# Kernel optimization log

Measured on AMD Instinct MI355X. Metric: run time of the kernel, lower is better.

The kernel has to match this reference:

```python
import jax, jax.numpy as jnp
import numpy as np

EMBED_DIM = 128
NUM_HEADS = 4
WIN = (7, 7)
N = WIN[0] * WIN[1]  # 49
NW = 64              # windows per image
B = 128              # batch of images
SCALE = (EMBED_DIM // NUM_HEADS) ** -0.5


def _relative_position_index():
    coords = np.stack(np.meshgrid(np.arange(WIN[0]), np.arange(WIN[1]), indexing='ij'))
    cf = coords.reshape(2, -1)                       # [2, N]
    rel = cf[:, :, None] - cf[:, None, :]            # [2, N, N]
    rel = rel.transpose(1, 2, 0).astype(np.int64)    # [N, N, 2]
    rel[..., 0] += WIN[0] - 1
    rel[..., 0] *= 2 * WIN[1] - 1
    rel[..., 1] += WIN[1] - 1
    return rel.sum(-1).reshape(-1)                   # [N*N]


def setup_inputs() -> dict:
    key = jax.random.key(0)
    ks = jax.random.split(key, 6)
    C = EMBED_DIM
    x = jax.random.normal(ks[0], (NW * B, N, C), dtype=jnp.float32)
    mask = jnp.zeros((NW, N, N), dtype=jnp.float32)
    qkv_w = jax.random.normal(ks[1], (3 * C, C), dtype=jnp.float32) * (C ** -0.5)
    qkv_b = jnp.zeros((3 * C,), dtype=jnp.float32)
    proj_w = jax.random.normal(ks[2], (C, C), dtype=jnp.float32) * (C ** -0.5)
    proj_b = jnp.zeros((C,), dtype=jnp.float32)
    bias_table = jax.random.normal(ks[3], ((2 * WIN[0] - 1) * (2 * WIN[1] - 1), NUM_HEADS), dtype=jnp.float32) * 0.02
    rel_index = jnp.asarray(_relative_position_index(), dtype=jnp.int32)
    return {"x": x, "mask": mask, "qkv_w": qkv_w, "qkv_b": qkv_b,
            "proj_w": proj_w, "proj_b": proj_b, "bias_table": bias_table,
            "rel_index": rel_index}


def reference(x, mask, qkv_w, qkv_b, proj_w, proj_b, bias_table, rel_index):
    nwb, n, c = x.shape
    nh, ch = NUM_HEADS, c // NUM_HEADS
    qkv = x @ qkv_w.T + qkv_b                               # [nwb, n, 3c]
    qkv = qkv.reshape(nwb, n, 3, nh, ch)
    q, k, v = (jnp.moveaxis(qkv, (2, 3), (0, 2))[i] for i in range(3))  # each [nwb, nh, n, ch]
    attn = jnp.einsum('whik,whjk->whij', q * SCALE, k)      # [nwb, nh, n, n]
    # relative position bias: gather then reshape to [1, nh, n, n]
    bias = bias_table[rel_index].reshape(n, n, nh).transpose(2, 0, 1)[None]
    attn = attn + bias
    if mask is not None:
        nw = mask.shape[0]
        attn = attn.reshape(nwb // nw, nw, nh, n, n) + mask[None, :, None]
        attn = attn.reshape(nwb, nh, n, n)
    attn = jax.nn.softmax(attn, axis=-1)
    out = jnp.einsum('whij,whjd->whid', attn, v)            # [nwb, nh, n, ch]
    out = out.transpose(0, 2, 1, 3).reshape(nwb, n, c)
    return out @ proj_w.T + proj_b
```

## Files before the change

kernel.cpp:

```cpp
#include <hip/hip_runtime.h>

typedef __bf16 bf16x8 __attribute__((ext_vector_type(8)));
typedef float  f32x4  __attribute__((ext_vector_type(4)));

#define NTOK  49
#define CDIM  128
#define QK_SCALE 0.17677669529663687f

#define XS 136
#define QS 264
#define VS 72
#define PS 64

#define WQKV_OFF  0
#define WPROJ_OFF 98304
#define BIASF_OFF 131072

__global__ void prep_kernel(const float* __restrict__ qkv_w,
                            const float* __restrict__ proj_w,
                            const float* __restrict__ bias_table,
                            const int*   __restrict__ rel_index,
                            __bf16* __restrict__ wqkv,
                            __bf16* __restrict__ wproj,
                            float*  __restrict__ biasf) {
    int t = blockIdx.x * 256 + threadIdx.x;
    if (t < 384 * 128) wqkv[t]  = (__bf16)qkv_w[t];
    if (t < 128 * 128) wproj[t] = (__bf16)proj_w[t];
    if (t < 4 * 2401) {
        int h = t / 2401, ij = t % 2401;
        biasf[t] = bias_table[rel_index[ij] * 4 + h];
    }
}

__launch_bounds__(256, 2)
__global__ void winattn_kernel(const float* __restrict__ x,
                               const float* __restrict__ mask,
                               const float* __restrict__ qkv_b,
                               const float* __restrict__ proj_b,
                               const __bf16* __restrict__ wqkv,
                               const __bf16* __restrict__ wproj,
                               const float* __restrict__ biasf,
                               float* __restrict__ out) {
    __shared__ __bf16 lds_x[64 * XS];
    __shared__ __bf16 lds_qkv[64 * QS];
    __shared__ __bf16 lds_vt[128 * VS];
    __bf16* lds_p = lds_qkv;

    const int tid  = threadIdx.x;
    const int w    = blockIdx.x;
    const int wave = tid >> 6;
    const int lane = tid & 63;
    const int quad = lane >> 4;
    const int l16  = lane & 15;

    {
        int row = tid >> 2;
        int c0  = (tid & 3) * 32;
        __align__(16) __bf16 tmp[32];
        if (row < NTOK) {
            const float4* src = (const float4*)(x + ((size_t)w * NTOK + row) * CDIM + c0);
            #pragma unroll
            for (int i = 0; i < 8; ++i) {
                float4 f = src[i];
                tmp[i*4+0] = (__bf16)f.x; tmp[i*4+1] = (__bf16)f.y;
                tmp[i*4+2] = (__bf16)f.z; tmp[i*4+3] = (__bf16)f.w;
            }
        } else {
            #pragma unroll
            for (int i = 0; i < 32; ++i) tmp[i] = (__bf16)0.0f;
        }
        bf16x8* dst = (bf16x8*)&lds_x[row * XS + c0];
        #pragma unroll
        for (int i = 0; i < 4; ++i) dst[i] = *(bf16x8*)&tmp[i*8];
    }
    __syncthreads();

    #pragma unroll
    for (int half = 0; half < 2; ++half) {
        f32x4 acc[3][4];
        #pragma unroll
        for (int a = 0; a < 3; ++a)
            #pragma unroll
            for (int b = 0; b < 4; ++b) acc[a][b] = (f32x4){0.f,0.f,0.f,0.f};

        #pragma unroll
        for (int kt = 0; kt < 4; ++kt) {
            bf16x8 a4[4];
            #pragma unroll
            for (int mt = 0; mt < 4; ++mt)
                a4[mt] = *(bf16x8*)&lds_x[(mt*16 + l16) * XS + kt*32 + quad*8];
            #pragma unroll
            for (int ntl = 0; ntl < 3; ++ntl) {
                int o = (wave*6 + half*3 + ntl) * 16 + l16;
                bf16x8 bf = *(const bf16x8*)(wqkv + (size_t)o * CDIM + kt*32 + quad*8);
                #pragma unroll
                for (int mt = 0; mt < 4; ++mt)
                    acc[ntl][mt] = __builtin_amdgcn_mfma_f32_16x16x32_bf16(
                        a4[mt], bf, acc[ntl][mt], 0, 0, 0);
            }
        }
        #pragma unroll
        for (int ntl = 0; ntl < 3; ++ntl) {
            int o = (wave*6 + half*3 + ntl) * 16 + l16;
            float b = qkv_b[o];
            #pragma unroll
            for (int mt = 0; mt < 4; ++mt) {
                #pragma unroll
                for (int r = 0; r < 4; ++r) {
                    int row = mt*16 + quad*4 + r;
                    float v = acc[ntl][mt][r] + b;
                    if (o < 128)       lds_qkv[row * QS + o] = (__bf16)(v * QK_SCALE);
                    else if (o < 256)  lds_qkv[row * QS + o] = (__bf16)v;
                    else               lds_vt[(o - 256) * VS + row] = (__bf16)v;
                }
            }
        }
    }
    __syncthreads();

    {
        const int h = wave;
        bf16x8 bk[4];
        #pragma unroll
        for (int nt = 0; nt < 4; ++nt)
            bk[nt] = *(bf16x8*)&lds_qkv[(nt*16 + l16) * QS + 128 + h*32 + quad*8];

        f32x4 s[4][4];
        #pragma unroll
        for (int mt = 0; mt < 4; ++mt) {
            bf16x8 aq = *(bf16x8*)&lds_qkv[(mt*16 + l16) * QS + h*32 + quad*8];
            #pragma unroll
            for (int nt = 0; nt < 4; ++nt) {
                f32x4 z = (f32x4){0.f,0.f,0.f,0.f};
                s[mt][nt] = __builtin_amdgcn_mfma_f32_16x16x32_bf16(aq, bk[nt], z, 0, 0, 0);
            }
        }

        const float* bh = biasf + h * 2401;
        const float* mh = mask + (size_t)(w & 63) * 2401;
        #pragma unroll
        for (int mt = 0; mt < 4; ++mt) {
            #pragma unroll
            for (int r = 0; r < 4; ++r) {
                int i = mt*16 + quad*4 + r;
                float v[4];
                #pragma unroll
                for (int nt = 0; nt < 4; ++nt) {
                    int j = nt*16 + l16;
                    float t = s[mt][nt][r];
                    if (j < NTOK) { if (i < NTOK) t += bh[i*49 + j] + mh[i*49 + j]; }
                    else t = -1e30f;
                    v[nt] = t;
                }
                float mx = fmaxf(fmaxf(v[0], v[1]), fmaxf(v[2], v[3]));
                mx = fmaxf(mx, __shfl_xor(mx, 1, 64));
                mx = fmaxf(mx, __shfl_xor(mx, 2, 64));
                mx = fmaxf(mx, __shfl_xor(mx, 4, 64));
                mx = fmaxf(mx, __shfl_xor(mx, 8, 64));
                float e[4], sum = 0.f;
                #pragma unroll
                for (int nt = 0; nt < 4; ++nt) { e[nt] = __expf(v[nt] - mx); sum += e[nt]; }
                sum += __shfl_xor(sum, 1, 64);
                sum += __shfl_xor(sum, 2, 64);
                sum += __shfl_xor(sum, 4, 64);
                sum += __shfl_xor(sum, 8, 64);
                float inv = 1.0f / sum;
                #pragma unroll
                for (int nt = 0; nt < 4; ++nt) s[mt][nt][r] = e[nt] * inv;
            }
        }
        __syncthreads();
        #pragma unroll
        for (int mt = 0; mt < 4; ++mt)
            #pragma unroll
            for (int r = 0; r < 4; ++r)
                #pragma unroll
                for (int nt = 0; nt < 4; ++nt)
                    lds_p[((h << 6) + mt*16 + quad*4 + r) * PS + nt*16 + l16] =
                        (__bf16)s[mt][nt][r];
    }
    __syncthreads();

    {
        const int h = wave;
        bf16x8 bv[2][2];
        #pragma unroll
        for (int nv = 0; nv < 2; ++nv)
            #pragma unroll
            for (int kt = 0; kt < 2; ++kt)
                bv[nv][kt] = *(bf16x8*)&lds_vt[(h*32 + nv*16 + l16) * VS + kt*32 + quad*8];

        f32x4 oacc[4][2];
        #pragma unroll
        for (int a = 0; a < 4; ++a)
            #pragma unroll
            for (int b = 0; b < 2; ++b) oacc[a][b] = (f32x4){0.f,0.f,0.f,0.f};

        #pragma unroll
        for (int mt = 0; mt < 4; ++mt)
            #pragma unroll
            for (int kt = 0; kt < 2; ++kt) {
                bf16x8 ap = *(bf16x8*)&lds_p[((h << 6) + mt*16 + l16) * PS + kt*32 + quad*8];
                #pragma unroll
                for (int nv = 0; nv < 2; ++nv)
                    oacc[mt][nv] = __builtin_amdgcn_mfma_f32_16x16x32_bf16(
                        ap, bv[nv][kt], oacc[mt][nv], 0, 0, 0);
            }

        #pragma unroll
        for (int mt = 0; mt < 4; ++mt)
            #pragma unroll
            for (int nv = 0; nv < 2; ++nv)
                #pragma unroll
                for (int r = 0; r < 4; ++r) {
                    int row = mt*16 + quad*4 + r;
                    lds_x[row * XS + h*32 + nv*16 + l16] = (__bf16)oacc[mt][nv][r];
                }
    }
    __syncthreads();

    #pragma unroll
    for (int ntl = 0; ntl < 2; ++ntl) {
        int o = (wave*2 + ntl) * 16 + l16;
        f32x4 acc[4];
        #pragma unroll
        for (int a = 0; a < 4; ++a) acc[a] = (f32x4){0.f,0.f,0.f,0.f};
        #pragma unroll
        for (int kt = 0; kt < 4; ++kt) {
            bf16x8 bf = *(const bf16x8*)(wproj + (size_t)o * CDIM + kt*32 + quad*8);
            #pragma unroll
            for (int mt = 0; mt < 4; ++mt) {
                bf16x8 af = *(bf16x8*)&lds_x[(mt*16 + l16) * XS + kt*32 + quad*8];
                acc[mt] = __builtin_amdgcn_mfma_f32_16x16x32_bf16(af, bf, acc[mt], 0, 0, 0);
            }
        }
        float pb = proj_b[o];
        #pragma unroll
        for (int mt = 0; mt < 4; ++mt)
            #pragma unroll
            for (int r = 0; r < 4; ++r) {
                int row = mt*16 + quad*4 + r;
                if (row < NTOK)
                    out[((size_t)w * NTOK + row) * CDIM + o] = acc[mt][r] + pb;
            }
    }
}

extern "C" void kernel_launch(void* const* d_in, const int* in_sizes, int n_in,
                              void* d_out, int out_size, void* d_ws, size_t ws_size,
                              hipStream_t stream) {
    const float* x          = (const float*)d_in[0];
    const float* mask       = (const float*)d_in[1];
    const float* qkv_w      = (const float*)d_in[2];
    const float* qkv_b      = (const float*)d_in[3];
    const float* proj_w     = (const float*)d_in[4];
    const float* proj_b     = (const float*)d_in[5];
    const float* bias_table = (const float*)d_in[6];
    const int*   rel_index  = (const int*)d_in[7];

    __bf16* wqkv  = (__bf16*)((char*)d_ws + WQKV_OFF);
    __bf16* wproj = (__bf16*)((char*)d_ws + WPROJ_OFF);
    float*  biasf = (float*)((char*)d_ws + BIASF_OFF);

    int nwb = in_sizes[0] / (NTOK * CDIM);

    prep_kernel<<<192, 256, 0, stream>>>(qkv_w, proj_w, bias_table, rel_index,
                                         wqkv, wproj, biasf);
    winattn_kernel<<<nwb, 256, 0, stream>>>(x, mask, qkv_b, proj_b,
                                            wqkv, wproj, biasf, (float*)d_out);
}
```

Before: 639.2 us.

## Keep Q/K/P in registers, premerge bias+mask in bf16, raise occupancy

Restructures the window-attention kernel so each wave computes its head's Q and K projections transposed and keeps them in registers as MFMA operands. The scores are computed as K·Q^T with 16x16x16 MFMAs, so the softmax probabilities feed the P·V MFMA straight from registers. This removes the large lds_qkv buffer and the LDS round trips for Q, K and P. The prep kernel now builds a padded bf16 table that folds the relative-position bias, mask and -inf padding together per window, head and position, replacing the separate fp32 bias and mask loads. Launch bounds rise to 4 blocks per CU, which risks register pressure and costs a larger, bf16-rounded bias/mask table.

```diff
diff --git a/kernel.cpp b/kernel.cpp
--- a/kernel.cpp
+++ b/kernel.cpp
@@ -1,6 +1,8 @@
 #include <hip/hip_runtime.h>
 
 typedef __bf16 bf16x8 __attribute__((ext_vector_type(8)));
+typedef __bf16 bf16x4 __attribute__((ext_vector_type(4)));
+typedef short  short4v __attribute__((ext_vector_type(4)));
 typedef float  f32x4  __attribute__((ext_vector_type(4)));
 
 #define NTOK  49
@@ -8,47 +10,60 @@
 #define QK_SCALE 0.17677669529663687f
 
 #define XS 136
-#define QS 264
 #define VS 72
-#define PS 64
 
 #define WQKV_OFF  0
 #define WPROJ_OFF 98304
-#define BIASF_OFF 131072
+#define BM_OFF    131072
+
+#define MFMA32(A,B,C) __builtin_amdgcn_mfma_f32_16x16x32_bf16(A,B,C,0,0,0)
+#define MFMA16(A,B,C) __builtin_amdgcn_mfma_f32_16x16x16bf16_1k(A,B,C,0,0,0)
 
 __global__ void prep_kernel(const float* __restrict__ qkv_w,
                             const float* __restrict__ proj_w,
                             const float* __restrict__ bias_table,
                             const int*   __restrict__ rel_index,
+                            const float* __restrict__ mask,
                             __bf16* __restrict__ wqkv,
                             __bf16* __restrict__ wproj,
-                            float*  __restrict__ biasf) {
+                            __bf16* __restrict__ bm) {
     int t = blockIdx.x * 256 + threadIdx.x;
     if (t < 384 * 128) wqkv[t]  = (__bf16)qkv_w[t];
     if (t < 128 * 128) wproj[t] = (__bf16)proj_w[t];
-    if (t < 4 * 2401) {
-        int h = t / 2401, ij = t % 2401;
-        biasf[t] = bias_table[rel_index[ij] * 4 + h];
-    }
-}
-
-__launch_bounds__(256, 2)
+    {
+        int i  = t & 63;
+        int j  = (t >> 6) & 63;
+        int h  = (t >> 12) & 3;
+        int wq = t >> 14;
+        float v;
+        if (j >= NTOK)      v = -1e30f;
+        else if (i >= NTOK) v = 0.0f;
+        else v = bias_table[rel_index[i * 49 + j] * 4 + h] + mask[wq * 2401 + i * 49 + j];
+        bm[t] = (__bf16)v;
+    }
+}
+
+static __device__ __forceinline__ short4v cvt_scale(f32x4 v, float b, float sc) {
+    bf16x4 r;
+    #pragma unroll
+    for (int i = 0; i < 4; ++i) r[i] = (__bf16)((v[i] + b) * sc);
+    return __builtin_bit_cast(short4v, r);
+}
+
+__launch_bounds__(256, 4)
 __global__ void winattn_kernel(const float* __restrict__ x,
-                               const float* __restrict__ mask,
                                const float* __restrict__ qkv_b,
                                const float* __restrict__ proj_b,
                                const __bf16* __restrict__ wqkv,
                                const __bf16* __restrict__ wproj,
-                               const float* __restrict__ biasf,
+                               const __bf16* __restrict__ bm,
                                float* __restrict__ out) {
     __shared__ __bf16 lds_x[64 * XS];
-    __shared__ __bf16 lds_qkv[64 * QS];
     __shared__ __bf16 lds_vt[128 * VS];
-    __bf16* lds_p = lds_qkv;
 
     const int tid  = threadIdx.x;
     const int w    = blockIdx.x;
-    const int wave = tid >> 6;
+    const int h    = tid >> 6;
     const int lane = tid & 63;
     const int quad = lane >> 4;
     const int l16  = lane & 15;
@@ -75,153 +90,166 @@
     }
     __syncthreads();
 
-    #pragma unroll
-    for (int half = 0; half < 2; ++half) {
-        f32x4 acc[3][4];
-        #pragma unroll
-        for (int a = 0; a < 3; ++a)
+    short4v qf[2][4], kf[2][4];
+
+    #pragma unroll
+    for (int sub = 0; sub < 3; ++sub) {
+        const int obase = sub * 128 + h * 32;
+        f32x4 acc[2][4];
+        #pragma unroll
+        for (int a = 0; a < 2; ++a)
             #pragma unroll
             for (int b = 0; b < 4; ++b) acc[a][b] = (f32x4){0.f,0.f,0.f,0.f};
 
         #pragma unroll
         for (int kt = 0; kt < 4; ++kt) {
-            bf16x8 a4[4];
-            #pragma unroll
-            for (int mt = 0; mt < 4; ++mt)
-                a4[mt] = *(bf16x8*)&lds_x[(mt*16 + l16) * XS + kt*32 + quad*8];
-            #pragma unroll
-            for (int ntl = 0; ntl < 3; ++ntl) {
-                int o = (wave*6 + half*3 + ntl) * 16 + l16;
-                bf16x8 bf = *(const bf16x8*)(wqkv + (size_t)o * CDIM + kt*32 + quad*8);
-                #pragma unroll
-                for (int mt = 0; mt < 4; ++mt)
-                    acc[ntl][mt] = __builtin_amdgcn_mfma_f32_16x16x32_bf16(
-                        a4[mt], bf, acc[ntl][mt], 0, 0, 0);
-            }
-        }
-        #pragma unroll
-        for (int ntl = 0; ntl < 3; ++ntl) {
-            int o = (wave*6 + half*3 + ntl) * 16 + l16;
-            float b = qkv_b[o];
-            #pragma unroll
-            for (int mt = 0; mt < 4; ++mt) {
-                #pragma unroll
-                for (int r = 0; r < 4; ++r) {
-                    int row = mt*16 + quad*4 + r;
-                    float v = acc[ntl][mt][r] + b;
-                    if (o < 128)       lds_qkv[row * QS + o] = (__bf16)(v * QK_SCALE);
-                    else if (o < 256)  lds_qkv[row * QS + o] = (__bf16)v;
-                    else               lds_vt[(o - 256) * VS + row] = (__bf16)v;
+            bf16x8 aw[2];
+            #pragma unroll
+            for (int mt = 0; mt < 2; ++mt)
+                aw[mt] = *(const bf16x8*)(wqkv + (size_t)(obase + mt*16 + l16) * CDIM + kt*32 + quad*8);
+            #pragma unroll
+            for (int nt = 0; nt < 4; ++nt) {
+                bf16x8 xb = *(bf16x8*)&lds_x[(nt*16 + l16) * XS + kt*32 + quad*8];
+                #pragma unroll
+                for (int mt = 0; mt < 2; ++mt)
+                    acc[mt][nt] = MFMA32(aw[mt], xb, acc[mt][nt]);
+            }
+        }
+
+        float bias[2][4];
+        #pragma unroll
+        for (int mt = 0; mt < 2; ++mt)
+            #pragma unroll
+            for (int r = 0; r < 4; ++r)
+                bias[mt][r] = qkv_b[obase + mt*16 + quad*4 + r];
+
+        if (sub == 0) {
+            #pragma unroll
+            for (int mt = 0; mt < 2; ++mt)
+                #pragma unroll
+                for (int nt = 0; nt < 4; ++nt) {
+                    bf16x4 r4;
+                    #pragma unroll
+                    for (int r = 0; r < 4; ++r)
+                        r4[r] = (__bf16)((acc[mt][nt][r] + bias[mt][r]) * QK_SCALE);
+                    qf[mt][nt] = __builtin_bit_cast(short4v, r4);
                 }
-            }
-        }
-    }
+        } else if (sub == 1) {
+            #pragma unroll
+            for (int mt = 0; mt < 2; ++mt)
+                #pragma unroll
+                for (int nt = 0; nt < 4; ++nt) {
+                    bf16x4 r4;
+                    #pragma unroll
+                    for (int r = 0; r < 4; ++r)
+                        r4[r] = (__bf16)(acc[mt][nt][r] + bias[mt][r]);
+                    kf[mt][nt] = __builtin_bit_cast(short4v, r4);
+                }
+        } else {
+            #pragma unroll
+            for (int mt = 0; mt < 2; ++mt)
+                #pragma unroll
+                for (int nt = 0; nt < 4; ++nt)
+                    #pragma unroll
+                    for (int r = 0; r < 4; ++r)
+                        lds_vt[(h*32 + mt*16 + quad*4 + r) * VS + nt*16 + l16] =
+                            (__bf16)(acc[mt][nt][r] + bias[mt][r]);
+        }
+    }
+
+    f32x4 s[4][4];
+    #pragma unroll
+    for (int jt = 0; jt < 4; ++jt)
+        #pragma unroll
+        for (int it = 0; it < 4; ++it) {
+            f32x4 z = (f32x4){0.f,0.f,0.f,0.f};
+            z = MFMA16(kf[0][jt], qf[0][it], z);
+            s[jt][it] = MFMA16(kf[1][jt], qf[1][it], z);
+        }
+
+    {
+        const __bf16* bmw = bm + (((size_t)(w & 63) * 4 + h) << 12);
+        #pragma unroll
+        for (int jt = 0; jt < 4; ++jt)
+            #pragma unroll
+            for (int r = 0; r < 4; ++r) {
+                int j = jt*16 + quad*4 + r;
+                #pragma unroll
+                for (int it = 0; it < 4; ++it)
+                    s[jt][it][r] += (float)bmw[j*64 + it*16 + l16];
+            }
+    }
+
+    short4v pf[4][4];
+    #pragma unroll
+    for (int it = 0; it < 4; ++it) {
+        float mx = -1e30f;
+        #pragma unroll
+        for (int jt = 0; jt < 4; ++jt)
+            #pragma unroll
+            for (int r = 0; r < 4; ++r) mx = fmaxf(mx, s[jt][it][r]);
+        mx = fmaxf(mx, __shfl_xor(mx, 16, 64));
+        mx = fmaxf(mx, __shfl_xor(mx, 32, 64));
+        float sum = 0.f;
+        #pragma unroll
+        for (int jt = 0; jt < 4; ++jt)
+            #pragma unroll
+            for (int r = 0; r < 4; ++r) {
+                float e = __expf(s[jt][it][r] - mx);
+                s[jt][it][r] = e;
+                sum += e;
+            }
+        sum += __shfl_xor(sum, 16, 64);
+        sum += __shfl_xor(sum, 32, 64);
+        float inv = 1.0f / sum;
+        #pragma unroll
+        for (int jt = 0; jt < 4; ++jt) {
+            bf16x4 r4;
+            #pragma unroll
+            for (int r = 0; r < 4; ++r) r4[r] = (__bf16)(s[jt][it][r] * inv);
+            pf[jt][it] = __builtin_bit_cast(short4v, r4);
+        }
+    }
+
     __syncthreads();
 
     {
-        const int h = wave;
-        bf16x8 bk[4];
-        #pragma unroll
-        for (int nt = 0; nt < 4; ++nt)
-            bk[nt] = *(bf16x8*)&lds_qkv[(nt*16 + l16) * QS + 128 + h*32 + quad*8];
-
-        f32x4 s[4][4];
-        #pragma unroll
-        for (int mt = 0; mt < 4; ++mt) {
-            bf16x8 aq = *(bf16x8*)&lds_qkv[(mt*16 + l16) * QS + h*32 + quad*8];
-            #pragma unroll
-            for (int nt = 0; nt < 4; ++nt) {
-                f32x4 z = (f32x4){0.f,0.f,0.f,0.f};
-                s[mt][nt] = __builtin_amdgcn_mfma_f32_16x16x32_bf16(aq, bk[nt], z, 0, 0, 0);
-            }
-        }
-
-        const float* bh = biasf + h * 2401;
-        const float* mh = mask + (size_t)(w & 63) * 2401;
-        #pragma unroll
-        for (int mt = 0; mt < 4; ++mt) {
-            #pragma unroll
-            for (int r = 0; r < 4; ++r) {
-                int i = mt*16 + quad*4 + r;
-                float v[4];
-                #pragma unroll
-                for (int nt = 0; nt < 4; ++nt) {
-                    int j = nt*16 + l16;
-                    float t = s[mt][nt][r];
-                    if (j < NTOK) { if (i < NTOK) t += bh[i*49 + j] + mh[i*49 + j]; }
-                    else t = -1e30f;
-                    v[nt] = t;
-                }
-                float mx = fmaxf(fmaxf(v[0], v[1]), fmaxf(v[2], v[3]));
-                mx = fmaxf(mx, __shfl_xor(mx, 1, 64));
-                mx = fmaxf(mx, __shfl_xor(mx, 2, 64));
-                mx = fmaxf(mx, __shfl_xor(mx, 4, 64));
-                mx = fmaxf(mx, __shfl_xor(mx, 8, 64));
-                float e[4], sum = 0.f;
-                #pragma unroll
-                for (int nt = 0; nt < 4; ++nt) { e[nt] = __expf(v[nt] - mx); sum += e[nt]; }
-                sum += __shfl_xor(sum, 1, 64);
-                sum += __shfl_xor(sum, 2, 64);
-                sum += __shfl_xor(sum, 4, 64);
-                sum += __shfl_xor(sum, 8, 64);
-                float inv = 1.0f / sum;
-                #pragma unroll
-                for (int nt = 0; nt < 4; ++nt) s[mt][nt][r] = e[nt] * inv;
-            }
-        }
-        __syncthreads();
-        #pragma unroll
-        for (int mt = 0; mt < 4; ++mt)
-            #pragma unroll
-            for (int r = 0; r < 4; ++r)
-                #pragma unroll
-                for (int nt = 0; nt < 4; ++nt)
-                    lds_p[((h << 6) + mt*16 + quad*4 + r) * PS + nt*16 + l16] =
-                        (__bf16)s[mt][nt][r];
+        short4v bv[2][4];
+        #pragma unroll
+        for (int nv = 0; nv < 2; ++nv)
+            #pragma unroll
+            for (int kt = 0; kt < 4; ++kt)
+                bv[nv][kt] = __builtin_bit_cast(short4v,
+                    *(bf16x4*)&lds_vt[(h*32 + nv*16 + l16) * VS + kt*16 + quad*4]);
+
+        f32x4 oacc[4][2];
+        #pragma unroll
+        for (int a = 0; a < 4; ++a)
+            #pragma unroll
+            for (int b = 0; b < 2; ++b) oacc[a][b] = (f32x4){0.f,0.f,0.f,0.f};
+
+        #pragma unroll
+        for (int it = 0; it < 4; ++it)
+            #pragma unroll
+            for (int kt = 0; kt < 4; ++kt)
+                #pragma unroll
+                for (int nv = 0; nv < 2; ++nv)
+                    oacc[it][nv] = MFMA16(pf[kt][it], bv[nv][kt], oacc[it][nv]);
+
+        #pragma unroll
+        for (int it = 0; it < 4; ++it)
+            #pragma unroll
+            for (int nv = 0; nv < 2; ++nv)
+                #pragma unroll
+                for (int r = 0; r < 4; ++r)
+                    lds_x[(it*16 + quad*4 + r) * XS + h*32 + nv*16 + l16] =
+                        (__bf16)oacc[it][nv][r];
     }
     __syncthreads();
 
-    {
-        const int h = wave;
-        bf16x8 bv[2][2];
-        #pragma unroll
-        for (int nv = 0; nv < 2; ++nv)
-            #pragma unroll
-            for (int kt = 0; kt < 2; ++kt)
-                bv[nv][kt] = *(bf16x8*)&lds_vt[(h*32 + nv*16 + l16) * VS + kt*32 + quad*8];
-
-        f32x4 oacc[4][2];
-        #pragma unroll
-        for (int a = 0; a < 4; ++a)
-            #pragma unroll
-            for (int b = 0; b < 2; ++b) oacc[a][b] = (f32x4){0.f,0.f,0.f,0.f};
-
-        #pragma unroll
-        for (int mt = 0; mt < 4; ++mt)
-            #pragma unroll
-            for (int kt = 0; kt < 2; ++kt) {
-                bf16x8 ap = *(bf16x8*)&lds_p[((h << 6) + mt*16 + l16) * PS + kt*32 + quad*8];
-                #pragma unroll
-                for (int nv = 0; nv < 2; ++nv)
-                    oacc[mt][nv] = __builtin_amdgcn_mfma_f32_16x16x32_bf16(
-                        ap, bv[nv][kt], oacc[mt][nv], 0, 0, 0);
-            }
-
-        #pragma unroll
-        for (int mt = 0; mt < 4; ++mt)
-            #pragma unroll
-            for (int nv = 0; nv < 2; ++nv)
-                #pragma unroll
-                for (int r = 0; r < 4; ++r) {
-                    int row = mt*16 + quad*4 + r;
-                    lds_x[row * XS + h*32 + nv*16 + l16] = (__bf16)oacc[mt][nv][r];
-                }
-    }
-    __syncthreads();
-
     #pragma unroll
     for (int ntl = 0; ntl < 2; ++ntl) {
-        int o = (wave*2 + ntl) * 16 + l16;
+        int o = (h*2 + ntl) * 16 + l16;
         f32x4 acc[4];
         #pragma unroll
         for (int a = 0; a < 4; ++a) acc[a] = (f32x4){0.f,0.f,0.f,0.f};
@@ -231,7 +259,7 @@
             #pragma unroll
             for (int mt = 0; mt < 4; ++mt) {
                 bf16x8 af = *(bf16x8*)&lds_x[(mt*16 + l16) * XS + kt*32 + quad*8];
-                acc[mt] = __builtin_amdgcn_mfma_f32_16x16x32_bf16(af, bf, acc[mt], 0, 0, 0);
+                acc[mt] = MFMA32(af, bf, acc[mt]);
             }
         }
         float pb = proj_b[o];
@@ -260,12 +288,12 @@
 
     __bf16* wqkv  = (__bf16*)((char*)d_ws + WQKV_OFF);
     __bf16* wproj = (__bf16*)((char*)d_ws + WPROJ_OFF);
-    float*  biasf = (float*)((char*)d_ws + BIASF_OFF);
+    __bf16* bm    = (__bf16*)((char*)d_ws + BM_OFF);
 
     int nwb = in_sizes[0] / (NTOK * CDIM);
 
-    prep_kernel<<<192, 256, 0, stream>>>(qkv_w, proj_w, bias_table, rel_index,
-                                         wqkv, wproj, biasf);
-    winattn_kernel<<<nwb, 256, 0, stream>>>(x, mask, qkv_b, proj_b,
-                                            wqkv, wproj, biasf, (float*)d_out);
-}
+    prep_kernel<<<4096, 256, 0, stream>>>(qkv_w, proj_w, bias_table, rel_index,
+                                          mask, wqkv, wproj, bm);
+    winattn_kernel<<<nwb, 256, 0, stream>>>(x, qkv_b, proj_b,
+                                            wqkv, wproj, bm, (float*)d_out);
+}
```

After: 669.2 us. 1.05x slower.
